# Kernel tuning notes

Hardware: AMD Instinct MI355X
Metric: run time of the kernel (lower is better)

The kernel has to match this reference:

```python
import jax, jax.numpy as jnp
import numpy as np

P_CHAN, P_FEAT = 7, 2
S_CHAN, S_FEAT = 2, 4
STATE_SIZE = 8
E, H = 32, 4
ACTIONS = 7
B = 131072


def _lin(x, w, b):
    return x @ w.T + b


def _ln(x, g, b):
    mu = jnp.mean(x, axis=-1, keepdims=True)
    var = jnp.var(x, axis=-1, keepdims=True)
    return (x - mu) * jax.lax.rsqrt(var + 1e-5) * g + b


def _encoder(x, qkv_w, qkv_b, o_w, o_b, g1, b1, f1w, f1b, f2w, f2b, g2, b2):
    # torch.nn.TransformerEncoderLayer, post-norm, relu, dropout=0
    Bn, S, Em = x.shape
    D = Em // H
    qkv = _lin(x, qkv_w, qkv_b)                      # [B,S,3E]
    q, k, v = jnp.split(qkv, 3, axis=-1)
    q = q.reshape(Bn, S, H, D).transpose(0, 2, 1, 3)  # [B,H,S,D]
    k = k.reshape(Bn, S, H, D).transpose(0, 2, 1, 3)
    v = v.reshape(Bn, S, H, D).transpose(0, 2, 1, 3)
    scores = jnp.einsum('bhsd,bhtd->bhst', q, k) * (1.0 / np.sqrt(D))
    att = jax.nn.softmax(scores, axis=-1)
    o = jnp.einsum('bhst,bhtd->bhsd', att, v).transpose(0, 2, 1, 3).reshape(Bn, S, Em)
    x = _ln(x + _lin(o, o_w, o_b), g1, b1)
    ff = _lin(jax.nn.relu(_lin(x, f1w, f1b)), f2w, f2b)
    return _ln(x + ff, g2, b2)


_BRANCH_NAMES = ['in_w', 'in_b', 'qkv_w', 'qkv_b', 'o_w', 'o_b', 'ln1_g', 'ln1_b',
                 'ff1_w', 'ff1_b', 'ff2_w', 'ff2_b', 'ln2_g', 'ln2_b', 'out_w', 'out_b']


def _branch_params(ks, feat, chan):
    def W(shape):
        s = 1.0 / np.sqrt(shape[-1])
        return jax.random.uniform(next(ks), shape, jnp.float32, -s, s)
    return [W((E, feat)), W((E,)), W((3 * E, E)), W((3 * E,)), W((E, E)), W((E,)),
            jnp.ones(E, jnp.float32), jnp.zeros(E, jnp.float32),
            W((E, E)), W((E,)), W((E, E)), W((E,)),
            jnp.ones(E, jnp.float32), jnp.zeros(E, jnp.float32),
            W((128, chan * E)), W((128,))]


def setup_inputs() -> dict:
    key = jax.random.key(0)
    ks = iter(jax.random.split(key, 64))
    def W(shape):
        s = 1.0 / np.sqrt(shape[-1])
        return jax.random.uniform(next(ks), shape, jnp.float32, -s, s)
    d = {'state': jax.random.normal(next(ks), (B, P_CHAN * P_FEAT + S_CHAN * S_FEAT + STATE_SIZE), jnp.float32)}
    d.update({f'pw_{n}': v for n, v in zip(_BRANCH_NAMES, _branch_params(ks, P_FEAT, P_CHAN))})
    d.update({f'sw_{n}': v for n, v in zip(_BRANCH_NAMES, _branch_params(ks, S_FEAT, S_CHAN))})
    d.update(dict(e_w=W((128, STATE_SIZE)), e_b=W((128,)),
                  d1_w=W((128, 384)), d1_b=W((128,)),
                  d2_w=W((128, 128)), d2_b=W((128,)),
                  pi_w=W((ACTIONS, 128)), pi_b=W((ACTIONS,)),
                  v_w=W((1, 128)), v_b=W((1,))))
    return d


def reference(state, pw_in_w, pw_in_b, pw_qkv_w, pw_qkv_b, pw_o_w, pw_o_b, pw_ln1_g, pw_ln1_b,
              pw_ff1_w, pw_ff1_b, pw_ff2_w, pw_ff2_b, pw_ln2_g, pw_ln2_b, pw_out_w, pw_out_b,
              sw_in_w, sw_in_b, sw_qkv_w, sw_qkv_b, sw_o_w, sw_o_b, sw_ln1_g, sw_ln1_b,
              sw_ff1_w, sw_ff1_b, sw_ff2_w, sw_ff2_b, sw_ln2_g, sw_ln2_b, sw_out_w, sw_out_b,
              e_w, e_b, d1_w, d1_b, d2_w, d2_b, pi_w, pi_b, v_w, v_b):
    Bn = state.shape[0]
    power, sword, ps = jnp.split(state, [P_CHAN * P_FEAT, P_CHAN * P_FEAT + S_CHAN * S_FEAT], axis=1)

    p = _lin(power.reshape(Bn * P_CHAN, P_FEAT), pw_in_w, pw_in_b).reshape(Bn, P_CHAN, E)
    p = _encoder(p, pw_qkv_w, pw_qkv_b, pw_o_w, pw_o_b, pw_ln1_g, pw_ln1_b,
                 pw_ff1_w, pw_ff1_b, pw_ff2_w, pw_ff2_b, pw_ln2_g, pw_ln2_b)
    p_emb = jax.nn.relu(_lin(p.reshape(Bn, -1), pw_out_w, pw_out_b))

    s = _lin(sword.reshape(Bn * S_CHAN, S_FEAT), sw_in_w, sw_in_b).reshape(Bn, S_CHAN, E)
    s = _encoder(s, sw_qkv_w, sw_qkv_b, sw_o_w, sw_o_b, sw_ln1_g, sw_ln1_b,
                 sw_ff1_w, sw_ff1_b, sw_ff2_w, sw_ff2_b, sw_ln2_g, sw_ln2_b)
    s_emb = jax.nn.relu(_lin(s.reshape(Bn, -1), sw_out_w, sw_out_b))

    st_emb = jax.nn.relu(_lin(ps, e_w, e_b))
    x = jnp.concatenate([p_emb, s_emb, st_emb], axis=1)  # [B,384]
    x = jax.nn.relu(_lin(x, d1_w, d1_b))
    x = jax.nn.relu(_lin(x, d2_w, d2_b))
    return jax.nn.softmax(_lin(x, pi_w, pi_b), axis=-1), _lin(x, v_w, v_b)
```

## Files before the change

### kernel.cpp

```cpp
#include <hip/hip_runtime.h>


typedef __bf16 bhalf;
typedef __bf16 bhalf4 __attribute__((ext_vector_type(4)));
typedef __bf16 bhalf8 __attribute__((ext_vector_type(8)));
typedef float f32x4 __attribute__((ext_vector_type(4)));
typedef float f32x2 __attribute__((ext_vector_type(2)));

#define DEV static __device__ __forceinline__

DEV f32x4 mfma16(bhalf8 a, bhalf8 b, f32x4 c) {
  return __builtin_amdgcn_mfma_f32_16x16x32_bf16(a, b, c, 0, 0, 0);
}

DEV int sxo(int row, int col) { return row * 32 + (col ^ ((row & 3) << 3)); }

struct Ptrs {
  const float* state;
  const float *p_g1, *p_b1, *p_f1b, *p_f2b, *p_g2, *p_b2, *p_out_b;
  const float *s_g1, *s_b1, *s_f1b, *s_f2b, *s_g2, *s_b2, *s_out_b;
  const float *d1_b, *d2_b, *pi_w, *pi_b, *v_w, *v_b;
  const bhalf *A_qp, *A_xp, *w_o, *w_f1, *w_f2, *w_out;
  const bhalf *A_qs, *A_xs, *w_o2, *w_f12, *w_f22, *w_out2;
  const bhalf *A_e, *w_d1, *w_d2;
  float* out;
};

struct PrepArgs {
  const float* src[10];
  int len[10];
  int dstOff[10];
  bhalf* dst;
};

__global__ void prep_convert(PrepArgs a) {
  int idx = blockIdx.x * blockDim.x + threadIdx.x;
  int off = 0;
#pragma unroll
  for (int i = 0; i < 10; ++i) {
    int n = a.len[i];
    if (idx >= off && idx < off + n) a.dst[a.dstOff[i] + idx - off] = (bhalf)a.src[i][idx - off];
    off += n;
  }
}

struct EffArgs {
  const float *p_qkv_w, *p_in_w, *p_in_b, *p_qkv_b, *p_o_b;
  const float *s_qkv_w, *s_in_w, *s_in_b, *s_qkv_b, *s_o_b;
  const float *e_w, *e_b;
  bhalf* dst;
};

__global__ void prep_eff(EffArgs a) {
  int tid = threadIdx.x;
  if (tid < 96) {
    const float* wq = a.p_qkv_w + tid * 32;
    float w0 = 0.f, w1 = 0.f, be = 0.f;
    for (int e = 0; e < 32; ++e) {
      w0 += wq[e] * a.p_in_w[e * 2];
      w1 += wq[e] * a.p_in_w[e * 2 + 1];
      be += wq[e] * a.p_in_b[e];
    }
    be += a.p_qkv_b[tid];
    bhalf* d = a.dst + tid * 32;
    for (int k = 0; k < 32; ++k) d[k] = (bhalf)0.f;
    d[0] = (bhalf)w0; d[1] = (bhalf)w1; d[2] = (bhalf)be;
  } else if (tid < 192) {
    int o = tid - 96;
    const float* wq = a.s_qkv_w + o * 32;
    float wf[4] = {0.f, 0.f, 0.f, 0.f}, be = 0.f;
    for (int e = 0; e < 32; ++e) {
      for (int f = 0; f < 4; ++f) wf[f] += wq[e] * a.s_in_w[e * 4 + f];
      be += wq[e] * a.s_in_b[e];
    }
    be += a.s_qkv_b[o];
    bhalf* d = a.dst + 35840 + o * 32;
    for (int k = 0; k < 32; ++k) d[k] = (bhalf)0.f;
    for (int f = 0; f < 4; ++f) d[f] = (bhalf)wf[f];
    d[4] = (bhalf)be;
  } else if (tid < 224) {
    int e = tid - 192;
    bhalf* d = a.dst + 3072 + e * 32;
    for (int k = 0; k < 32; ++k) d[k] = (bhalf)0.f;
    d[0] = (bhalf)a.p_in_w[e * 2];
    d[1] = (bhalf)a.p_in_w[e * 2 + 1];
    d[2] = (bhalf)(a.p_in_b[e] + a.p_o_b[e]);
  } else if (tid < 256) {
    int e = tid - 224;
    bhalf* d = a.dst + 38912 + e * 32;
    for (int k = 0; k < 32; ++k) d[k] = (bhalf)0.f;
    for (int f = 0; f < 4; ++f) d[f] = (bhalf)a.s_in_w[e * 4 + f];
    d[4] = (bhalf)(a.s_in_b[e] + a.s_o_b[e]);
  } else if (tid < 384) {
    int o = tid - 256;
    bhalf* d = a.dst + 51200 + o * 32;
    for (int k = 0; k < 32; ++k) d[k] = (bhalf)0.f;
    for (int k = 0; k < 8; ++k) d[k] = (bhalf)a.e_w[o * 8 + k];
    d[8] = (bhalf)a.e_b[o];
  }
}

DEV void p1_tile(const Ptrs& P, bhalf* s_q, int tile, int s0, int l15, int lq,
                 f32x4& cx0, f32x4& cx1) {
  const bool sw = tile >= 14;
  bhalf8 bf;
#pragma unroll
  for (int k = 0; k < 8; ++k) bf[k] = (bhalf)0.f;
  if (lq == 0) {
    int s = (tile & 1) * 16 + l15;
    const float* st = &P.state[(size_t)(s0 + s) * 30];
    if (!sw) {
      int t = tile >> 1;
      f32x2 v = *(const f32x2*)(st + 2 * t);
      bf[0] = (bhalf)v[0]; bf[1] = (bhalf)v[1]; bf[2] = (bhalf)1.0f;
    } else {
      int ts = (tile - 14) >> 1;
      f32x2 v0 = *(const f32x2*)(st + 14 + 4 * ts);
      f32x2 v1 = *(const f32x2*)(st + 16 + 4 * ts);
      bf[0] = (bhalf)v0[0]; bf[1] = (bhalf)v0[1];
      bf[2] = (bhalf)v1[0]; bf[3] = (bhalf)v1[1];
      bf[4] = (bhalf)1.0f;
    }
  }
  const bhalf* Aq = sw ? P.A_qs : P.A_qp;
  const bhalf* Ax = sw ? P.A_xs : P.A_xp;
  const int row = tile * 16 + l15;
#pragma unroll
  for (int n = 0; n < 6; ++n) {
    f32x4 c = {0.f, 0.f, 0.f, 0.f};
    c = mfma16(*(const bhalf8*)&Aq[(n * 16 + l15) * 32 + lq * 8], bf, c);
    bhalf4 o;
#pragma unroll
    for (int j = 0; j < 4; ++j) o[j] = (bhalf)c[j];
    *(bhalf4*)&s_q[row * 104 + n * 16 + lq * 4] = o;
  }
  cx0 = f32x4{0.f, 0.f, 0.f, 0.f};
  cx1 = f32x4{0.f, 0.f, 0.f, 0.f};
  cx0 = mfma16(*(const bhalf8*)&Ax[l15 * 32 + lq * 8], bf, cx0);
  cx1 = mfma16(*(const bhalf8*)&Ax[(16 + l15) * 32 + lq * 8], bf, cx1);
}

template <int T>
DEV bhalf8 attn_head(const bhalf* qkv, int rowbase, int a, int s, int h) {
  const bhalf* base = &qkv[(rowbase + s) * 104 + h * 8];
  const int rstep = 32 * 104;
  bhalf8 kf[T];
#pragma unroll
  for (int b = 0; b < T; ++b) kf[b] = *(const bhalf8*)(base + b * rstep + 32);
  bhalf8 qv = *(const bhalf8*)(base + a * rstep);
  float q[8];
#pragma unroll
  for (int i = 0; i < 8; ++i) q[i] = (float)qv[i];
  float sc[T];
  float mx = -1e30f;
#pragma unroll
  for (int b = 0; b < T; ++b) {
    float d = 0.f;
#pragma unroll
    for (int i = 0; i < 8; ++i) d += q[i] * (float)kf[b][i];
    d *= 0.35355339059327378f;
    sc[b] = d;
    mx = fmaxf(mx, d);
  }
  bhalf8 vf[T];
#pragma unroll
  for (int b = 0; b < T; ++b) vf[b] = *(const bhalf8*)(base + b * rstep + 64);
  float sum = 0.f;
#pragma unroll
  for (int b = 0; b < T; ++b) { sc[b] = __expf(sc[b] - mx); sum += sc[b]; }
  float inv = 1.f / sum;
  float o[8] = {0.f, 0.f, 0.f, 0.f, 0.f, 0.f, 0.f, 0.f};
#pragma unroll
  for (int b = 0; b < T; ++b) {
    float w = sc[b] * inv;
#pragma unroll
    for (int i = 0; i < 8; ++i) o[i] += w * (float)vf[b][i];
  }
  bhalf8 ov;
#pragma unroll
  for (int i = 0; i < 8; ++i) ov[i] = (bhalf)o[i];
  return ov;
}

template <int T>
DEV void enc_tile(const bhalf* s_q, bhalf* s_x, int tile, int l15, int lq,
                  f32x4 c0, f32x4 c1,
                  const bhalf* wo, const bhalf* wf1, const bhalf* wf2,
                  const float* g1, const float* b1, const float* f1b,
                  const float* f2b, const float* g2, const float* b2) {
  const int rowbase = (T == 7) ? 0 : 224;
  const int a = (T == 7) ? (tile >> 1) : ((tile - 14) >> 1);
  const int s = (tile & 1) * 16 + l15;
  bhalf8 ov = attn_head<T>(s_q, rowbase, a, s, lq);
  const int row = tile * 16 + l15;
  c0 = mfma16(*(const bhalf8*)&wo[l15 * 32 + lq * 8], ov, c0);
  c1 = mfma16(*(const bhalf8*)&wo[(16 + l15) * 32 + lq * 8], ov, c1);
  float sum = 0.f, ss = 0.f;
#pragma unroll
  for (int j = 0; j < 4; ++j) { sum += c0[j] + c1[j]; ss += c0[j] * c0[j] + c1[j] * c1[j]; }
  sum += __shfl_xor(sum, 16); sum += __shfl_xor(sum, 32);
  ss += __shfl_xor(ss, 16); ss += __shfl_xor(ss, 32);
  float mu = sum * 0.03125f;
  float rs = rsqrtf(ss * 0.03125f - mu * mu + 1e-5f);
  f32x4 gg0 = *(const f32x4*)&g1[lq * 4], gg1 = *(const f32x4*)&g1[16 + lq * 4];
  f32x4 hb0 = *(const f32x4*)&b1[lq * 4], hb1 = *(const f32x4*)&b1[16 + lq * 4];
  float xn[8];
#pragma unroll
  for (int j = 0; j < 4; ++j) {
    xn[j] = (c0[j] - mu) * rs * gg0[j] + hb0[j];
    xn[4 + j] = (c1[j] - mu) * rs * gg1[j] + hb1[j];
  }
  bhalf4 p0, p1;
#pragma unroll
  for (int j = 0; j < 4; ++j) { p0[j] = (bhalf)xn[j]; p1[j] = (bhalf)xn[4 + j]; }
  *(bhalf4*)&s_x[sxo(row, lq * 4)] = p0;
  *(bhalf4*)&s_x[sxo(row, 16 + lq * 4)] = p1;
  bhalf8 bfr = *(const bhalf8*)&s_x[sxo(row, lq * 8)];
  c0 = f32x4{0.f, 0.f, 0.f, 0.f};
  c1 = f32x4{0.f, 0.f, 0.f, 0.f};
  c0 = mfma16(*(const bhalf8*)&wf1[l15 * 32 + lq * 8], bfr, c0);
  c1 = mfma16(*(const bhalf8*)&wf1[(16 + l15) * 32 + lq * 8], bfr, c1);
  f32x4 fb0 = *(const f32x4*)&f1b[lq * 4], fb1 = *(const f32x4*)&f1b[16 + lq * 4];
#pragma unroll
  for (int j = 0; j < 4; ++j) {
    p0[j] = (bhalf)fmaxf(c0[j] + fb0[j], 0.f);
    p1[j] = (bhalf)fmaxf(c1[j] + fb1[j], 0.f);
  }
  *(bhalf4*)&s_x[sxo(row, lq * 4)] = p0;
  *(bhalf4*)&s_x[sxo(row, 16 + lq * 4)] = p1;
  bfr = *(const bhalf8*)&s_x[sxo(row, lq * 8)];
  f32x4 f20 = *(const f32x4*)&f2b[lq * 4], f21 = *(const f32x4*)&f2b[16 + lq * 4];
#pragma unroll
  for (int j = 0; j < 4; ++j) { c0[j] = xn[j] + f20[j]; c1[j] = xn[4 + j] + f21[j]; }
  c0 = mfma16(*(const bhalf8*)&wf2[l15 * 32 + lq * 8], bfr, c0);
  c1 = mfma16(*(const bhalf8*)&wf2[(16 + l15) * 32 + lq * 8], bfr, c1);
  sum = 0.f; ss = 0.f;
#pragma unroll
  for (int j = 0; j < 4; ++j) { sum += c0[j] + c1[j]; ss += c0[j] * c0[j] + c1[j] * c1[j]; }
  sum += __shfl_xor(sum, 16); sum += __shfl_xor(sum, 32);
  ss += __shfl_xor(ss, 16); ss += __shfl_xor(ss, 32);
  mu = sum * 0.03125f;
  rs = rsqrtf(ss * 0.03125f - mu * mu + 1e-5f);
  f32x4 g20 = *(const f32x4*)&g2[lq * 4], g21 = *(const f32x4*)&g2[16 + lq * 4];
  f32x4 b20 = *(const f32x4*)&b2[lq * 4], b21 = *(const f32x4*)&b2[16 + lq * 4];
#pragma unroll
  for (int j = 0; j < 4; ++j) {
    p0[j] = (bhalf)((c0[j] - mu) * rs * g20[j] + b20[j]);
    p1[j] = (bhalf)((c1[j] - mu) * rs * g21[j] + b21[j]);
  }
  *(bhalf4*)&s_x[sxo(row, lq * 4)] = p0;
  *(bhalf4*)&s_x[sxo(row, 16 + lq * 4)] = p1;
}

__launch_bounds__(512, 4)
__global__ void aac_main(Ptrs P) {
  __shared__ __align__(16) bhalf s_x[288 * 32];
  __shared__ __align__(16) bhalf s_q[288 * 104];

  bhalf* xcat = s_q;
  bhalf* h1 = s_q + 13056;
  float* h2 = (float*)(s_q + 17408);

  const int tid = threadIdx.x;
  const int wave = tid >> 6, lane = tid & 63;
  const int l15 = lane & 15, lq = lane >> 4;
  const int s0 = blockIdx.x * 32;

  f32x4 xA0, xA1, xB0, xB1, xC0, xC1;
  p1_tile(P, s_q, wave, s0, l15, lq, xA0, xA1);
  p1_tile(P, s_q, wave + 8, s0, l15, lq, xB0, xB1);
  if (wave < 2) p1_tile(P, s_q, 16 + wave, s0, l15, lq, xC0, xC1);
  __syncthreads();

  enc_tile<7>(s_q, s_x, wave, l15, lq, xA0, xA1,
              P.w_o, P.w_f1, P.w_f2, P.p_g1, P.p_b1, P.p_f1b, P.p_f2b, P.p_g2, P.p_b2);
  if (wave < 6) {
    enc_tile<7>(s_q, s_x, wave + 8, l15, lq, xB0, xB1,
                P.w_o, P.w_f1, P.w_f2, P.p_g1, P.p_b1, P.p_f1b, P.p_f2b, P.p_g2, P.p_b2);
  } else {
    enc_tile<2>(s_q, s_x, wave + 8, l15, lq, xB0, xB1,
                P.w_o2, P.w_f12, P.w_f22, P.s_g1, P.s_b1, P.s_f1b, P.s_f2b, P.s_g2, P.s_b2);
  }
  if (wave < 2) {
    enc_tile<2>(s_q, s_x, 16 + wave, l15, lq, xC0, xC1,
                P.w_o2, P.w_f12, P.w_f22, P.s_g1, P.s_b1, P.s_f1b, P.s_f2b, P.s_g2, P.s_b2);
  }
  __syncthreads();

#pragma unroll
  for (int k = 0; k < 2; ++k) {
    int f = wave + 8 * k;
    int n = f >> 1, m = f & 1;
    f32x4 c = {0.f, 0.f, 0.f, 0.f};
#pragma unroll
    for (int t = 0; t < 7; ++t) {
      bhalf8 a = *(const bhalf8*)&P.w_out[(n * 16 + l15) * 224 + t * 32 + lq * 8];
      bhalf8 b = *(const bhalf8*)&s_x[sxo(t * 32 + m * 16 + l15, lq * 8)];
      c = mfma16(a, b, c);
    }
    int oc = n * 16 + lq * 4;
    f32x4 bias = *(const f32x4*)&P.p_out_b[oc];
    bhalf4 o;
#pragma unroll
    for (int j = 0; j < 4; ++j) o[j] = (bhalf)fmaxf(c[j] + bias[j], 0.f);
    *(bhalf4*)&xcat[(m * 16 + l15) * 408 + oc] = o;
  }
#pragma unroll
  for (int k = 0; k < 2; ++k) {
    int g = wave + 8 * k;
    int n = g >> 1, m = g & 1;
    f32x4 c = {0.f, 0.f, 0.f, 0.f};
#pragma unroll
    for (int t = 0; t < 2; ++t) {
      bhalf8 a = *(const bhalf8*)&P.w_out2[(n * 16 + l15) * 64 + t * 32 + lq * 8];
      bhalf8 b = *(const bhalf8*)&s_x[sxo(224 + t * 32 + m * 16 + l15, lq * 8)];
      c = mfma16(a, b, c);
    }
    int oc = n * 16 + lq * 4;
    f32x4 bias = *(const f32x4*)&P.s_out_b[oc];
    bhalf4 o;
#pragma unroll
    for (int j = 0; j < 4; ++j) o[j] = (bhalf)fmaxf(c[j] + bias[j], 0.f);
    *(bhalf4*)&xcat[(m * 16 + l15) * 408 + 128 + oc] = o;
  }
#pragma unroll
  for (int k = 0; k < 2; ++k) {
    int g = wave + 8 * k;
    int n = g >> 1, m = g & 1;
    int s = m * 16 + l15;
    bhalf8 bf;
#pragma unroll
    for (int kk = 0; kk < 8; ++kk) bf[kk] = (bhalf)0.f;
    if (lq == 0) {
      const float* st = &P.state[(size_t)(s0 + s) * 30 + 22];
#pragma unroll
      for (int kk = 0; kk < 4; ++kk) {
        f32x2 v = *(const f32x2*)(st + 2 * kk);
        bf[2 * kk] = (bhalf)v[0];
        bf[2 * kk + 1] = (bhalf)v[1];
      }
    } else if (lq == 1) {
      bf[0] = (bhalf)1.0f;
    }
    bhalf8 a = *(const bhalf8*)&P.A_e[(n * 16 + l15) * 32 + lq * 8];
    f32x4 c = {0.f, 0.f, 0.f, 0.f};
    c = mfma16(a, bf, c);
    bhalf4 o;
#pragma unroll
    for (int j = 0; j < 4; ++j) o[j] = (bhalf)fmaxf(c[j], 0.f);
    *(bhalf4*)&xcat[s * 408 + 256 + n * 16 + lq * 4] = o;
  }
  __syncthreads();

#pragma unroll
  for (int m = 0; m < 2; ++m) {
    int n = wave;
    f32x4 c = {0.f, 0.f, 0.f, 0.f};
#pragma unroll
    for (int ks = 0; ks < 12; ++ks) {
      bhalf8 a = *(const bhalf8*)&P.w_d1[(n * 16 + l15) * 384 + ks * 32 + lq * 8];
      bhalf8 b = *(const bhalf8*)&xcat[(m * 16 + l15) * 408 + ks * 32 + lq * 8];
      c = mfma16(a, b, c);
    }
    int oc = n * 16 + lq * 4;
    f32x4 bias = *(const f32x4*)&P.d1_b[oc];
    bhalf4 o;
#pragma unroll
    for (int j = 0; j < 4; ++j) o[j] = (bhalf)fmaxf(c[j] + bias[j], 0.f);
    *(bhalf4*)&h1[(m * 16 + l15) * 136 + oc] = o;
  }
  __syncthreads();

#pragma unroll
  for (int m = 0; m < 2; ++m) {
    int n = wave;
    f32x4 c = {0.f, 0.f, 0.f, 0.f};
#pragma unroll
    for (int ks = 0; ks < 4; ++ks) {
      bhalf8 a = *(const bhalf8*)&P.w_d2[(n * 16 + l15) * 128 + ks * 32 + lq * 8];
      bhalf8 b = *(const bhalf8*)&h1[(m * 16 + l15) * 136 + ks * 32 + lq * 8];
      c = mfma16(a, b, c);
    }
    int oc = n * 16 + lq * 4;
    f32x4 bias = *(const f32x4*)&P.d2_b[oc];
    f32x4 o;
#pragma unroll
    for (int j = 0; j < 4; ++j) o[j] = fmaxf(c[j] + bias[j], 0.f);
    *(f32x4*)&h2[(m * 16 + l15) * 140 + oc] = o;
  }
  __syncthreads();

  if (tid < 256) {
    int s = tid >> 3, o = tid & 7;
    const float* wrow = (o < 7) ? &P.pi_w[o * 128] : P.v_w;
    const float* hrow = &h2[s * 140];
    float acc = (o < 7) ? P.pi_b[o] : P.v_b[0];
#pragma unroll
    for (int k = 0; k < 32; ++k) {
      f32x4 wv = *(const f32x4*)&wrow[k * 4];
      f32x4 hv = *(const f32x4*)&hrow[k * 4];
#pragma unroll
      for (int j = 0; j < 4; ++j) acc += wv[j] * hv[j];
    }
    float xm = (o < 7) ? acc : -1e30f;
#pragma unroll
    for (int m = 1; m < 8; m <<= 1) xm = fmaxf(xm, __shfl_xor(xm, m));
    float e = (o < 7) ? __expf(acc - xm) : 0.f;
    float se = e;
#pragma unroll
    for (int m = 1; m < 8; m <<= 1) se += __shfl_xor(se, m);
    if (o < 7) P.out[(size_t)(s0 + s) * 7 + o] = e / se;
    else       P.out[917504 + s0 + s] = acc;
  }
}

extern "C" void kernel_launch(void* const* d_in, const int* in_sizes, int n_in,
                              void* d_out, int out_size, void* d_ws, size_t ws_size,
                              hipStream_t stream) {
  (void)in_sizes; (void)n_in; (void)out_size; (void)ws_size;
  const float* const* in = (const float* const*)d_in;
  bhalf* wbf = (bhalf*)d_ws;

  PrepArgs pa;
  const int srcIdx[10] = {5, 9, 11, 15, 21, 25, 27, 31, 35, 37};
  const int lens[10] = {1024, 1024, 1024, 28672, 1024, 1024, 1024, 8192, 49152, 16384};
  const int dsts[10] = {4096, 5120, 6144, 7168, 39936, 40960, 41984, 43008, 55296, 104448};
  for (int i = 0; i < 10; ++i) { pa.src[i] = in[srcIdx[i]]; pa.len[i] = lens[i]; pa.dstOff[i] = dsts[i]; }
  pa.dst = wbf;
  hipLaunchKernelGGL(prep_convert, dim3(424), dim3(256), 0, stream, pa);

  EffArgs ea;
  ea.p_qkv_w = in[3]; ea.p_in_w = in[1]; ea.p_in_b = in[2]; ea.p_qkv_b = in[4]; ea.p_o_b = in[6];
  ea.s_qkv_w = in[19]; ea.s_in_w = in[17]; ea.s_in_b = in[18]; ea.s_qkv_b = in[20]; ea.s_o_b = in[22];
  ea.e_w = in[33]; ea.e_b = in[34];
  ea.dst = wbf;
  hipLaunchKernelGGL(prep_eff, dim3(1), dim3(384), 0, stream, ea);

  Ptrs P;
  P.state = in[0];
  P.p_g1 = in[7];  P.p_b1 = in[8];  P.p_f1b = in[10]; P.p_f2b = in[12];
  P.p_g2 = in[13]; P.p_b2 = in[14]; P.p_out_b = in[16];
  P.s_g1 = in[23]; P.s_b1 = in[24]; P.s_f1b = in[26]; P.s_f2b = in[28];
  P.s_g2 = in[29]; P.s_b2 = in[30]; P.s_out_b = in[32];
  P.d1_b = in[36]; P.d2_b = in[38];
  P.pi_w = in[39]; P.pi_b = in[40]; P.v_w = in[41]; P.v_b = in[42];
  P.A_qp = wbf;          P.A_xp = wbf + 3072;   P.w_o = wbf + 4096;
  P.w_f1 = wbf + 5120;   P.w_f2 = wbf + 6144;   P.w_out = wbf + 7168;
  P.A_qs = wbf + 35840;  P.A_xs = wbf + 38912;  P.w_o2 = wbf + 39936;
  P.w_f12 = wbf + 40960; P.w_f22 = wbf + 41984; P.w_out2 = wbf + 43008;
  P.A_e = wbf + 51200;   P.w_d1 = wbf + 55296;  P.w_d2 = wbf + 104448;
  P.out = (float*)d_out;

  hipLaunchKernelGGL(aac_main, dim3(4096), dim3(512), 0, stream, P);
}
```

Measured before the change: 284.8 us.

## Halve samples per block to 16, doubling grid and occupancy

Each block now processes 16 samples instead of 32, which halves shared memory use and raises launch bounds to allow 8 blocks per CU. The wave-to-tile mapping is rebuilt for 9 tiles: waves 0-6 handle power channels and wave 7 handles both sword channels. This should cut register and LDS pressure and improve latency hiding. In exchange, wave 7 carries extra load, every block re-reads the weights, and each MFMA weight fetch is reused over fewer samples.

```diff
diff --git a/kernel.cpp b/kernel.cpp
--- a/kernel.cpp
+++ b/kernel.cpp
@@ -102,19 +102,17 @@
 
 DEV void p1_tile(const Ptrs& P, bhalf* s_q, int tile, int s0, int l15, int lq,
                  f32x4& cx0, f32x4& cx1) {
-  const bool sw = tile >= 14;
+  const bool sw = tile >= 7;
   bhalf8 bf;
 #pragma unroll
   for (int k = 0; k < 8; ++k) bf[k] = (bhalf)0.f;
   if (lq == 0) {
-    int s = (tile & 1) * 16 + l15;
-    const float* st = &P.state[(size_t)(s0 + s) * 30];
+    const float* st = &P.state[(size_t)(s0 + l15) * 30];
     if (!sw) {
-      int t = tile >> 1;
-      f32x2 v = *(const f32x2*)(st + 2 * t);
+      f32x2 v = *(const f32x2*)(st + 2 * tile);
       bf[0] = (bhalf)v[0]; bf[1] = (bhalf)v[1]; bf[2] = (bhalf)1.0f;
     } else {
-      int ts = (tile - 14) >> 1;
+      int ts = tile - 7;
       f32x2 v0 = *(const f32x2*)(st + 14 + 4 * ts);
       f32x2 v1 = *(const f32x2*)(st + 16 + 4 * ts);
       bf[0] = (bhalf)v0[0]; bf[1] = (bhalf)v0[1];
@@ -143,7 +141,7 @@
 template <int T>
 DEV bhalf8 attn_head(const bhalf* qkv, int rowbase, int a, int s, int h) {
   const bhalf* base = &qkv[(rowbase + s) * 104 + h * 8];
-  const int rstep = 32 * 104;
+  const int rstep = 16 * 104;
   bhalf8 kf[T];
 #pragma unroll
   for (int b = 0; b < T; ++b) kf[b] = *(const bhalf8*)(base + b * rstep + 32);
@@ -183,15 +181,12 @@
 }
 
 template <int T>
-DEV void enc_tile(const bhalf* s_q, bhalf* s_x, int tile, int l15, int lq,
-                  f32x4 c0, f32x4 c1,
+DEV void enc_tile(const bhalf* s_q, bhalf* s_x, int tile, int a, int rowbase,
+                  int l15, int lq, f32x4 c0, f32x4 c1,
                   const bhalf* wo, const bhalf* wf1, const bhalf* wf2,
                   const float* g1, const float* b1, const float* f1b,
                   const float* f2b, const float* g2, const float* b2) {
-  const int rowbase = (T == 7) ? 0 : 224;
-  const int a = (T == 7) ? (tile >> 1) : ((tile - 14) >> 1);
-  const int s = (tile & 1) * 16 + l15;
-  bhalf8 ov = attn_head<T>(s_q, rowbase, a, s, lq);
+  bhalf8 ov = attn_head<T>(s_q, rowbase, a, l15, lq);
   const int row = tile * 16 + l15;
   c0 = mfma16(*(const bhalf8*)&wo[l15 * 32 + lq * 8], ov, c0);
   c1 = mfma16(*(const bhalf8*)&wo[(16 + l15) * 32 + lq * 8], ov, c1);
@@ -252,50 +247,44 @@
   *(bhalf4*)&s_x[sxo(row, 16 + lq * 4)] = p1;
 }
 
-__launch_bounds__(512, 4)
+__launch_bounds__(512, 8)
 __global__ void aac_main(Ptrs P) {
-  __shared__ __align__(16) bhalf s_x[288 * 32];
-  __shared__ __align__(16) bhalf s_q[288 * 104];
+  __shared__ __align__(16) bhalf s_x[144 * 32];
+  __shared__ __align__(16) bhalf s_q[144 * 104];
 
   bhalf* xcat = s_q;
-  bhalf* h1 = s_q + 13056;
-  float* h2 = (float*)(s_q + 17408);
+  bhalf* h1 = s_q + 6528;
+  float* h2 = (float*)(s_q + 8704);
 
   const int tid = threadIdx.x;
   const int wave = tid >> 6, lane = tid & 63;
   const int l15 = lane & 15, lq = lane >> 4;
-  const int s0 = blockIdx.x * 32;
-
-  f32x4 xA0, xA1, xB0, xB1, xC0, xC1;
+  const int s0 = blockIdx.x * 16;
+
+  f32x4 xA0, xA1;
+  f32x4 xB0 = {0.f, 0.f, 0.f, 0.f}, xB1 = {0.f, 0.f, 0.f, 0.f};
   p1_tile(P, s_q, wave, s0, l15, lq, xA0, xA1);
-  p1_tile(P, s_q, wave + 8, s0, l15, lq, xB0, xB1);
-  if (wave < 2) p1_tile(P, s_q, 16 + wave, s0, l15, lq, xC0, xC1);
+  if (wave == 7) p1_tile(P, s_q, 8, s0, l15, lq, xB0, xB1);
   __syncthreads();
 
-  enc_tile<7>(s_q, s_x, wave, l15, lq, xA0, xA1,
-              P.w_o, P.w_f1, P.w_f2, P.p_g1, P.p_b1, P.p_f1b, P.p_f2b, P.p_g2, P.p_b2);
-  if (wave < 6) {
-    enc_tile<7>(s_q, s_x, wave + 8, l15, lq, xB0, xB1,
+  if (wave < 7) {
+    enc_tile<7>(s_q, s_x, wave, wave, 0, l15, lq, xA0, xA1,
                 P.w_o, P.w_f1, P.w_f2, P.p_g1, P.p_b1, P.p_f1b, P.p_f2b, P.p_g2, P.p_b2);
   } else {
-    enc_tile<2>(s_q, s_x, wave + 8, l15, lq, xB0, xB1,
+    enc_tile<2>(s_q, s_x, 7, 0, 112, l15, lq, xA0, xA1,
                 P.w_o2, P.w_f12, P.w_f22, P.s_g1, P.s_b1, P.s_f1b, P.s_f2b, P.s_g2, P.s_b2);
-  }
-  if (wave < 2) {
-    enc_tile<2>(s_q, s_x, 16 + wave, l15, lq, xC0, xC1,
+    enc_tile<2>(s_q, s_x, 8, 1, 112, l15, lq, xB0, xB1,
                 P.w_o2, P.w_f12, P.w_f22, P.s_g1, P.s_b1, P.s_f1b, P.s_f2b, P.s_g2, P.s_b2);
   }
   __syncthreads();
 
-#pragma unroll
-  for (int k = 0; k < 2; ++k) {
-    int f = wave + 8 * k;
-    int n = f >> 1, m = f & 1;
+  {
+    int n = wave;
     f32x4 c = {0.f, 0.f, 0.f, 0.f};
 #pragma unroll
     for (int t = 0; t < 7; ++t) {
       bhalf8 a = *(const bhalf8*)&P.w_out[(n * 16 + l15) * 224 + t * 32 + lq * 8];
-      bhalf8 b = *(const bhalf8*)&s_x[sxo(t * 32 + m * 16 + l15, lq * 8)];
+      bhalf8 b = *(const bhalf8*)&s_x[sxo(t * 16 + l15, lq * 8)];
       c = mfma16(a, b, c);
     }
     int oc = n * 16 + lq * 4;
@@ -303,36 +292,23 @@
     bhalf4 o;
 #pragma unroll
     for (int j = 0; j < 4; ++j) o[j] = (bhalf)fmaxf(c[j] + bias[j], 0.f);
-    *(bhalf4*)&xcat[(m * 16 + l15) * 408 + oc] = o;
-  }
-#pragma unroll
-  for (int k = 0; k < 2; ++k) {
-    int g = wave + 8 * k;
-    int n = g >> 1, m = g & 1;
-    f32x4 c = {0.f, 0.f, 0.f, 0.f};
+    *(bhalf4*)&xcat[l15 * 408 + oc] = o;
+    c = f32x4{0.f, 0.f, 0.f, 0.f};
 #pragma unroll
     for (int t = 0; t < 2; ++t) {
       bhalf8 a = *(const bhalf8*)&P.w_out2[(n * 16 + l15) * 64 + t * 32 + lq * 8];
-      bhalf8 b = *(const bhalf8*)&s_x[sxo(224 + t * 32 + m * 16 + l15, lq * 8)];
+      bhalf8 b = *(const bhalf8*)&s_x[sxo(112 + t * 16 + l15, lq * 8)];
       c = mfma16(a, b, c);
     }
-    int oc = n * 16 + lq * 4;
-    f32x4 bias = *(const f32x4*)&P.s_out_b[oc];
-    bhalf4 o;
+    bias = *(const f32x4*)&P.s_out_b[oc];
 #pragma unroll
     for (int j = 0; j < 4; ++j) o[j] = (bhalf)fmaxf(c[j] + bias[j], 0.f);
-    *(bhalf4*)&xcat[(m * 16 + l15) * 408 + 128 + oc] = o;
-  }
-#pragma unroll
-  for (int k = 0; k < 2; ++k) {
-    int g = wave + 8 * k;
-    int n = g >> 1, m = g & 1;
-    int s = m * 16 + l15;
+    *(bhalf4*)&xcat[l15 * 408 + 128 + oc] = o;
     bhalf8 bf;
 #pragma unroll
     for (int kk = 0; kk < 8; ++kk) bf[kk] = (bhalf)0.f;
     if (lq == 0) {
-      const float* st = &P.state[(size_t)(s0 + s) * 30 + 22];
+      const float* st = &P.state[(size_t)(s0 + l15) * 30 + 22];
 #pragma unroll
       for (int kk = 0; kk < 4; ++kk) {
         f32x2 v = *(const f32x2*)(st + 2 * kk);
@@ -343,23 +319,21 @@
       bf[0] = (bhalf)1.0f;
     }
     bhalf8 a = *(const bhalf8*)&P.A_e[(n * 16 + l15) * 32 + lq * 8];
-    f32x4 c = {0.f, 0.f, 0.f, 0.f};
+    c = f32x4{0.f, 0.f, 0.f, 0.f};
     c = mfma16(a, bf, c);
-    bhalf4 o;
 #pragma unroll
     for (int j = 0; j < 4; ++j) o[j] = (bhalf)fmaxf(c[j], 0.f);
-    *(bhalf4*)&xcat[s * 408 + 256 + n * 16 + lq * 4] = o;
+    *(bhalf4*)&xcat[l15 * 408 + 256 + oc] = o;
   }
   __syncthreads();
 
-#pragma unroll
-  for (int m = 0; m < 2; ++m) {
+  {
     int n = wave;
     f32x4 c = {0.f, 0.f, 0.f, 0.f};
 #pragma unroll
     for (int ks = 0; ks < 12; ++ks) {
       bhalf8 a = *(const bhalf8*)&P.w_d1[(n * 16 + l15) * 384 + ks * 32 + lq * 8];
-      bhalf8 b = *(const bhalf8*)&xcat[(m * 16 + l15) * 408 + ks * 32 + lq * 8];
+      bhalf8 b = *(const bhalf8*)&xcat[l15 * 408 + ks * 32 + lq * 8];
       c = mfma16(a, b, c);
     }
     int oc = n * 16 + lq * 4;
@@ -367,18 +341,17 @@
     bhalf4 o;
 #pragma unroll
     for (int j = 0; j < 4; ++j) o[j] = (bhalf)fmaxf(c[j] + bias[j], 0.f);
-    *(bhalf4*)&h1[(m * 16 + l15) * 136 + oc] = o;
+    *(bhalf4*)&h1[l15 * 136 + oc] = o;
   }
   __syncthreads();
 
-#pragma unroll
-  for (int m = 0; m < 2; ++m) {
+  {
     int n = wave;
     f32x4 c = {0.f, 0.f, 0.f, 0.f};
 #pragma unroll
     for (int ks = 0; ks < 4; ++ks) {
       bhalf8 a = *(const bhalf8*)&P.w_d2[(n * 16 + l15) * 128 + ks * 32 + lq * 8];
-      bhalf8 b = *(const bhalf8*)&h1[(m * 16 + l15) * 136 + ks * 32 + lq * 8];
+      bhalf8 b = *(const bhalf8*)&h1[l15 * 136 + ks * 32 + lq * 8];
       c = mfma16(a, b, c);
     }
     int oc = n * 16 + lq * 4;
@@ -386,11 +359,11 @@
     f32x4 o;
 #pragma unroll
     for (int j = 0; j < 4; ++j) o[j] = fmaxf(c[j] + bias[j], 0.f);
-    *(f32x4*)&h2[(m * 16 + l15) * 140 + oc] = o;
+    *(f32x4*)&h2[l15 * 140 + oc] = o;
   }
   __syncthreads();
 
-  if (tid < 256) {
+  if (tid < 128) {
     int s = tid >> 3, o = tid & 7;
     const float* wrow = (o < 7) ? &P.pi_w[o * 128] : P.v_w;
     const float* hrow = &h2[s * 140];
@@ -451,5 +424,5 @@
   P.A_e = wbf + 51200;   P.w_d1 = wbf + 55296;  P.w_d2 = wbf + 104448;
   P.out = (float*)d_out;
 
-  hipLaunchKernelGGL(aac_main, dim3(4096), dim3(512), 0, stream, P);
-}
+  hipLaunchKernelGGL(aac_main, dim3(8192), dim3(512), 0, stream, P);
+}
```

Result: slower. 364.6 us (+28.0%).
